# Kernel tuning notes

Measured on AMD Instinct MI355X. Metric: run time of the kernel, lower is better.

The kernel has to match this reference:

```python
import jax, jax.numpy as jnp
import numpy as np

B, S, D, H, L = 4, 2048, 512, 8, 4
DFF = 4 * D
CW = 128          # context_window
LS_MIN, LS_MAX = -6.0, 1.5


def setup_inputs() -> dict:
    key = jax.random.key(0)
    ks = jax.random.split(key, 10)
    s = 0.02
    p = lambda k, shape: jax.random.normal(k, shape, jnp.float32) * s
    return {
        "x": jax.random.normal(ks[0], (B, S, 2), jnp.float32),
        "W_in": p(ks[1], (D, 2)), "b_in": jnp.zeros((D,), jnp.float32),
        "pos": p(ks[2], (1, S, D)),
        "Wqkv": p(ks[3], (L, 3 * D, D)), "bqkv": jnp.zeros((L, 3 * D), jnp.float32),
        "Wo": p(ks[4], (L, D, D)), "bo": jnp.zeros((L, D), jnp.float32),
        "W1": p(ks[5], (L, DFF, D)), "b1": jnp.zeros((L, DFF), jnp.float32),
        "W2": p(ks[6], (L, D, DFF)), "b2": jnp.zeros((L, D), jnp.float32),
        "ln1_g": jnp.ones((L, D), jnp.float32), "ln1_b": jnp.zeros((L, D), jnp.float32),
        "ln2_g": jnp.ones((L, D), jnp.float32), "ln2_b": jnp.zeros((L, D), jnp.float32),
        "W_head": p(ks[7], (4, D)), "b_head": jnp.zeros((4,), jnp.float32),
    }


def _ln(x, g, b):
    m = x.mean(-1, keepdims=True)
    v = ((x - m) ** 2).mean(-1, keepdims=True)
    return (x - m) / jnp.sqrt(v + 1e-5) * g + b


def reference(x, W_in, b_in, pos, Wqkv, bqkv, Wo, bo, W1, b1, W2, b2,
              ln1_g, ln1_b, ln2_g, ln2_b, W_head, b_head):
    Bx, Sx, _ = x.shape
    h = x @ W_in.T + b_in + pos[:, :Sx, :]          # [B,S,D]
    idx = jnp.arange(Sx)
    # True = disallowed: future OR older than context window
    mask = (idx[None, :] > idx[:, None]) | (idx[None, :] < idx[:, None] - CW)
    dh = D // H
    scale = 1.0 / np.sqrt(dh).astype(np.float32)
    neg = jnp.float32(-1e30)
    for l in range(L):
        # self-attention (post-LN, as nn.TransformerEncoderLayer default)
        qkv = h @ Wqkv[l].T + bqkv[l]               # [B,S,3D]
        q, k, v = jnp.split(qkv, 3, axis=-1)
        q = q.reshape(Bx, Sx, H, dh)
        k = k.reshape(Bx, Sx, H, dh)
        v = v.reshape(Bx, Sx, H, dh)
        scores = jnp.einsum('bqhd,bkhd->bhqk', q, k) * scale
        scores = jnp.where(mask, neg, scores)
        attn = jax.nn.softmax(scores, axis=-1)
        o = jnp.einsum('bhqk,bkhd->bqhd', attn, v).reshape(Bx, Sx, D)
        h = _ln(h + o @ Wo[l].T + bo[l], ln1_g[l], ln1_b[l])
        # GELU FFN (exact erf gelu, torch default)
        ff = jax.nn.gelu(h @ W1[l].T + b1[l], approximate=False) @ W2[l].T + b2[l]
        h = _ln(h + ff, ln2_g[l], ln2_b[l])
    out = h @ W_head.T + b_head                     # [B,S,4]
    mu = out[..., :2]
    log_sigma = jnp.clip(out[..., 2:], LS_MIN, LS_MAX)
    return mu, log_sigma
```

## Files before the change

### kernel.cpp

```cpp
#include <hip/hip_runtime.h>
#include <hip/hip_bf16.h>
#include <math.h>

constexpr int Bc = 4;
constexpr int Sc = 2048;
constexpr int Dc = 512;
constexpr int Hc = 8;
constexpr int DHc = 64;
constexpr int Lc = 4;
constexpr int DFFc = 2048;
constexpr int Tc = Bc * Sc;
constexpr int QKVW = 3 * Dc;

typedef __attribute__((ext_vector_type(8))) short short8;
typedef __attribute__((ext_vector_type(4))) float f32x4;
typedef __attribute__((ext_vector_type(4))) float float4v;
typedef __attribute__((ext_vector_type(4))) unsigned int uint4v;

static __device__ __forceinline__ float u16tof(unsigned int u) {
  return __uint_as_float(u << 16);
}
static __device__ __forceinline__ unsigned short ftobf(float f) {
  __hip_bfloat16 h = __float2bfloat16(f);
  return *reinterpret_cast<unsigned short*>(&h);
}
static __device__ __forceinline__ void gload_lds16(const void* g, void* l) {
  __builtin_amdgcn_global_load_lds(
      (const __attribute__((address_space(1))) void*)g,
      (__attribute__((address_space(3))) void*)l, 16, 0, 0);
}

static __device__ __forceinline__ int swzK(int row, int col) {
  return row * 64 + ((((col >> 3) ^ (row & 7)) << 3) | (col & 7));
}
static __device__ __forceinline__ int swzW(int row, int col) {
  return row * 192 + ((((col >> 3) ^ (row & 7)) << 3) | (col & 7));
}

__global__ __launch_bounds__(256) void k_f2bf(const float* __restrict__ in,
                                              unsigned short* __restrict__ out,
                                              int n) {
  int i = blockIdx.x * 256 + threadIdx.x;
  if (i < n) out[i] = ftobf(in[i]);
}

__global__ __launch_bounds__(256) void k_embed(const float* __restrict__ x,
                                               const float* __restrict__ W_in,
                                               const float* __restrict__ b_in,
                                               const float* __restrict__ pos,
                                               float* __restrict__ h,
                                               unsigned short* __restrict__ hb) {
  int idx = blockIdx.x * 256 + threadIdx.x;
  int t = idx >> 9;
  int d = idx & 511;
  int s = t & (Sc - 1);
  float v = x[t * 2 + 0] * W_in[d * 2 + 0] + x[t * 2 + 1] * W_in[d * 2 + 1] +
            b_in[d] + pos[(size_t)s * Dc + d];
  h[idx] = v;
  hb[idx] = ftobf(v);
}

template <int MODE, int OUTBF>
__global__ __launch_bounds__(256, 4) void k_mgemm(const unsigned short* __restrict__ A,
                                                  const unsigned short* __restrict__ W,
                                                  const float* __restrict__ bias,
                                                  void* __restrict__ Cout,
                                                  int M, int N, int K) {
  __shared__ short SMEM[2][2][512 * 8];
  const int tid = threadIdx.x;
  const int lane = tid & 63;
  const int wid = tid >> 6;
  const int wm = wid >> 1;
  const int wn = wid & 1;

  const int nwg = gridDim.x * gridDim.y;
  const int bid = blockIdx.y * gridDim.x + blockIdx.x;
  const int swz = (bid & 7) * (nwg >> 3) + (bid >> 3);
  const int m0 = (swz / gridDim.x) * 128;
  const int n0 = (swz % gridDim.x) * 128;

  int r0S, c0S, r1S, c1S;
  {
    int p = tid;
    int rp = p >> 3, q = (p & 7) ^ (rp & 7);
    r0S = (rp << 1) | (q >> 2);
    c0S = q & 3;
    p = tid + 256;
    rp = p >> 3;
    q = (p & 7) ^ (rp & 7);
    r1S = (rp << 1) | (q >> 2);
    c1S = q & 3;
  }
  const unsigned short* a0p = A + (size_t)(m0 + r0S) * K + c0S * 8;
  const unsigned short* a1p = A + (size_t)(m0 + r1S) * K + c1S * 8;
  const unsigned short* b0p = W + (size_t)(n0 + r0S) * K + c0S * 8;
  const unsigned short* b1p = W + (size_t)(n0 + r1S) * K + c1S * 8;
  const int d0 = (tid & ~63) * 8;
  const int d1 = ((tid + 256) & ~63) * 8;

  f32x4 acc[4][4] = {};
  const int lr = lane & 15;
  const int chr = lane >> 4;

  gload_lds16(a0p, &SMEM[0][0][d0]);
  gload_lds16(a1p, &SMEM[0][0][d1]);
  gload_lds16(b0p, &SMEM[1][0][d0]);
  gload_lds16(b1p, &SMEM[1][0][d1]);
  __syncthreads();

  const int nsteps = K >> 5;
  int buf = 0;
  for (int s = 0; s < nsteps; ++s) {
    if (s + 1 < nsteps) {
      const int ko = (s + 1) << 5;
      gload_lds16(a0p + ko, &SMEM[0][buf ^ 1][d0]);
      gload_lds16(a1p + ko, &SMEM[0][buf ^ 1][d1]);
      gload_lds16(b0p + ko, &SMEM[1][buf ^ 1][d0]);
      gload_lds16(b1p + ko, &SMEM[1][buf ^ 1][d1]);
    }
    short8 af[4], bfr[4];
#pragma unroll
    for (int mi = 0; mi < 4; ++mi) {
      int row = wm * 64 + mi * 16 + lr;
      int rp = row >> 1;
      int p = rp * 8 + (((((row & 1) << 2) | chr)) ^ (rp & 7));
      af[mi] = *(const short8*)&SMEM[0][buf][p * 8];
    }
#pragma unroll
    for (int ni = 0; ni < 4; ++ni) {
      int row = wn * 64 + ni * 16 + lr;
      int rp = row >> 1;
      int p = rp * 8 + (((((row & 1) << 2) | chr)) ^ (rp & 7));
      bfr[ni] = *(const short8*)&SMEM[1][buf][p * 8];
    }
#pragma unroll
    for (int mi = 0; mi < 4; ++mi)
#pragma unroll
      for (int ni = 0; ni < 4; ++ni)
        acc[mi][ni] = __builtin_amdgcn_mfma_f32_16x16x32_bf16(
            af[mi], bfr[ni], acc[mi][ni], 0, 0, 0);
    __syncthreads();
    buf ^= 1;
  }

  float* cw = (float*)&SMEM[0][0][0] + wid * (16 * 68);
  const int cj = lane & 15;
  const int rj4 = (lane >> 4) * 4;
  const int rrd = lane >> 3;
  const int crd = (lane & 7) * 8;
#pragma unroll
  for (int mi = 0; mi < 4; ++mi) {
#pragma unroll
    for (int ni = 0; ni < 4; ++ni) {
      float bn = bias[n0 + wn * 64 + ni * 16 + cj];
#pragma unroll
      for (int j = 0; j < 4; ++j) {
        float v = acc[mi][ni][j] + bn;
        if (MODE == 2) v = 0.5f * v * (1.0f + erff(v * 0.70710678118654752f));
        cw[(rj4 + j) * 68 + ni * 16 + cj] = v;
      }
    }
    __builtin_amdgcn_sched_barrier(0);
#pragma unroll
    for (int t = 0; t < 2; ++t) {
      int rl = t * 8 + rrd;
      float4v v0 = *(const float4v*)&cw[rl * 68 + crd];
      float4v v1 = *(const float4v*)&cw[rl * 68 + crd + 4];
      size_t gbase = (size_t)(m0 + wm * 64 + mi * 16 + rl) * N +
                     (n0 + wn * 64 + crd);
      if (OUTBF) {
        unsigned int w0 = ftobf(v0[0]) | ((unsigned int)ftobf(v0[1]) << 16);
        unsigned int w1 = ftobf(v0[2]) | ((unsigned int)ftobf(v0[3]) << 16);
        unsigned int w2 = ftobf(v1[0]) | ((unsigned int)ftobf(v1[1]) << 16);
        unsigned int w3 = ftobf(v1[2]) | ((unsigned int)ftobf(v1[3]) << 16);
        uint4v pk = {w0, w1, w2, w3};
        *(uint4v*)&((unsigned short*)Cout)[gbase] = pk;
      } else {
        *(float4v*)&((float*)Cout)[gbase] = v0;
        *(float4v*)&((float*)Cout)[gbase + 4] = v1;
      }
    }
    __builtin_amdgcn_sched_barrier(0);
  }
}

__global__ __launch_bounds__(256, 3) void k_attn(const unsigned short* __restrict__ qkv,
                                                 unsigned short* __restrict__ o) {
  __shared__ unsigned short KPs[192 * 64];
  __shared__ unsigned short Vt[64 * 192];

  const int tid = threadIdx.x;
  const int lane = tid & 63;
  const int w = tid >> 6;
  const int idx = blockIdx.x;
  const int qb = idx & 31;
  const int hh = (idx >> 5) & 7;
  const int b = idx >> 8;
  const int q0 = qb * 64;
  const int kstart = max(0, q0 - 128);
  const int nk = q0 + 64 - kstart;

  for (int c = tid; c < nk * 8; c += 256) {
    int j = c >> 3, ch = c & 7;
    short8 kv = *(const short8*)&qkv[(size_t)(b * Sc + kstart + j) * QKVW + Dc + hh * DHc + ch * 8];
    *(short8*)&KPs[swzK(j, ch * 8)] = kv;
  }
  for (int c = tid; c < (nk >> 1) * 8; c += 256) {
    int jp = c >> 3, ch = c & 7;
    int j = jp * 2;
    const unsigned short* base =
        &qkv[(size_t)(b * Sc + kstart + j) * QKVW + 2 * Dc + hh * DHc + ch * 8];
    short8 v0 = *(const short8*)base;
    short8 v1 = *(const short8*)(base + QKVW);
#pragma unroll
    for (int i = 0; i < 8; ++i) {
      unsigned int pk = (unsigned short)v0[i] | ((unsigned int)(unsigned short)v1[i] << 16);
      *(unsigned int*)&Vt[swzW(ch * 8 + i, j)] = pk;
    }
  }
  if (nk < 192) {
    for (int c = tid; c < 64 * 64; c += 256) {
      int d = c >> 6, jo = c & 63;
      *(unsigned int*)&Vt[swzW(d, 64 + jo * 2)] = 0;
    }
  }

  const int qg = q0 + w * 16 + (lane & 15);
  const int kg8 = (lane >> 4) * 8;
  const unsigned short* qp = &qkv[(size_t)(b * Sc + qg) * QKVW + hh * DHc + kg8];
  short8 bq0 = *(const short8*)qp;
  short8 bq1 = *(const short8*)(qp + 32);
  __syncthreads();

  const int jb = max(0, q0 + w * 16 - 128) - kstart;

  f32x4 sacc[9];
#pragma unroll
  for (int t = 0; t < 9; ++t) {
    int key = jb + t * 16 + (lane & 15);
    short8 a0 = *(const short8*)&KPs[swzK(key, kg8)];
    short8 a1 = *(const short8*)&KPs[swzK(key, 32 + kg8)];
    f32x4 z = {0.f, 0.f, 0.f, 0.f};
    z = __builtin_amdgcn_mfma_f32_16x16x32_bf16(a0, bq0, z, 0, 0, 0);
    sacc[t] = __builtin_amdgcn_mfma_f32_16x16x32_bf16(a1, bq1, z, 0, 0, 0);
  }

  const int rj = (lane >> 4) * 4;
  float mx = -1e30f;
#pragma unroll
  for (int t = 0; t < 9; ++t) {
#pragma unroll
    for (int j = 0; j < 4; ++j) {
      int kglob = kstart + jb + t * 16 + rj + j;
      bool valid = (kglob <= qg) && (kglob + 128 >= qg);
      float s = valid ? sacc[t][j] * 0.125f : -1e30f;
      sacc[t][j] = s;
      mx = fmaxf(mx, s);
    }
  }
  mx = fmaxf(mx, __shfl_xor(mx, 16));
  mx = fmaxf(mx, __shfl_xor(mx, 32));
  float sum = 0.f;
#pragma unroll
  for (int t = 0; t < 9; ++t)
#pragma unroll
    for (int j = 0; j < 4; ++j) {
      float e = __expf(sacc[t][j] - mx);
      sacc[t][j] = e;
      sum += e;
    }
  sum += __shfl_xor(sum, 16);
  sum += __shfl_xor(sum, 32);
  const float inv = 1.0f / sum;

  __syncthreads();

  const int prow = w * 16 + (lane & 15);
#pragma unroll
  for (int t = 0; t < 9; ++t) {
    int c0 = jb + t * 16 + rj;
    unsigned int p0 = ftobf(sacc[t][0] * inv) |
                      ((unsigned int)ftobf(sacc[t][1] * inv) << 16);
    unsigned int p1 = ftobf(sacc[t][2] * inv) |
                      ((unsigned int)ftobf(sacc[t][3] * inv) << 16);
    *(unsigned int*)&KPs[swzW(prow, c0)] = p0;
    *(unsigned int*)&KPs[swzW(prow, c0 + 2)] = p1;
  }
  {
    int g2 = (lane >> 4) * 2;
    for (int col = g2; col < jb; col += 8)
      *(unsigned int*)&KPs[swzW(prow, col)] = 0;
    for (int col = jb + 144 + g2; col < 192; col += 8)
      *(unsigned int*)&KPs[swzW(prow, col)] = 0;
  }
  f32x4 oacc[4] = {};
#pragma unroll
  for (int kb = 0; kb < 6; ++kb) {
    short8 pa = *(const short8*)&KPs[swzW(prow, kb * 32 + kg8)];
#pragma unroll
    for (int dt = 0; dt < 4; ++dt) {
      short8 vb = *(const short8*)&Vt[swzW(dt * 16 + (lane & 15), kb * 32 + kg8)];
      oacc[dt] = __builtin_amdgcn_mfma_f32_16x16x32_bf16(pa, vb, oacc[dt], 0, 0, 0);
    }
  }
  const int cj = lane & 15;
#pragma unroll
  for (int j = 0; j < 4; ++j)
#pragma unroll
    for (int dt = 0; dt < 4; ++dt)
      o[(size_t)(b * Sc + q0 + w * 16 + rj + j) * Dc + hh * DHc + dt * 16 + cj] =
          ftobf(oacc[dt][j]);
}

__global__ __launch_bounds__(256) void k_lnr(float* __restrict__ h,
                                             const float* __restrict__ raw,
                                             const float* __restrict__ g,
                                             const float* __restrict__ bta,
                                             unsigned short* __restrict__ outb) {
  const int wid = threadIdx.x >> 6;
  const int lane = threadIdx.x & 63;
  const int t = blockIdx.x * 4 + wid;
  const float4v* hrow = (const float4v*)(h + (size_t)t * Dc);
  const float4v* rrow = (const float4v*)(raw + (size_t)t * Dc);
  float4v v[2];
  float sum = 0.0f, sq = 0.0f;
#pragma unroll
  for (int i = 0; i < 2; ++i) {
    float4v hv = hrow[lane + i * 64];
    float4v rv = rrow[lane + i * 64];
#pragma unroll
    for (int c = 0; c < 4; ++c) {
      float xv = rv[c] + hv[c];
      v[i][c] = xv;
      sum += xv;
      sq += xv * xv;
    }
  }
#pragma unroll
  for (int off = 32; off; off >>= 1) {
    sum += __shfl_xor(sum, off);
    sq += __shfl_xor(sq, off);
  }
  float m = sum * (1.0f / 512.0f);
  float var = sq * (1.0f / 512.0f) - m * m;
  float rstd = rsqrtf(var + 1e-5f);
  float4v* orow = (float4v*)(h + (size_t)t * Dc);
  unsigned int* brow = (unsigned int*)(outb + (size_t)t * Dc);
#pragma unroll
  for (int i = 0; i < 2; ++i) {
    int d4 = (lane + i * 64) * 4;
    float4v ov;
#pragma unroll
    for (int c = 0; c < 4; ++c)
      ov[c] = (v[i][c] - m) * rstd * g[d4 + c] + bta[d4 + c];
    orow[lane + i * 64] = ov;
    unsigned int p0 = ftobf(ov[0]) | ((unsigned int)ftobf(ov[1]) << 16);
    unsigned int p1 = ftobf(ov[2]) | ((unsigned int)ftobf(ov[3]) << 16);
    brow[(lane + i * 64) * 2] = p0;
    brow[(lane + i * 64) * 2 + 1] = p1;
  }
}

__global__ __launch_bounds__(256) void k_head(const float* __restrict__ h,
                                              const float* __restrict__ Wh,
                                              const float* __restrict__ bh,
                                              float* __restrict__ outp) {
  const int wid = threadIdx.x >> 6;
  const int lane = threadIdx.x & 63;
  const int t = blockIdx.x * 4 + wid;
  const float* row = h + (size_t)t * Dc;
  float a0 = 0, a1 = 0, a2 = 0, a3 = 0;
#pragma unroll
  for (int i = 0; i < 8; ++i) {
    int d = lane + i * 64;
    float xv = row[d];
    a0 += xv * Wh[0 * Dc + d];
    a1 += xv * Wh[1 * Dc + d];
    a2 += xv * Wh[2 * Dc + d];
    a3 += xv * Wh[3 * Dc + d];
  }
#pragma unroll
  for (int off = 32; off; off >>= 1) {
    a0 += __shfl_xor(a0, off);
    a1 += __shfl_xor(a1, off);
    a2 += __shfl_xor(a2, off);
    a3 += __shfl_xor(a3, off);
  }
  if (lane == 0) {
    outp[(size_t)t * 2 + 0] = a0 + bh[0];
    outp[(size_t)t * 2 + 1] = a1 + bh[1];
    outp[(size_t)Tc * 2 + (size_t)t * 2 + 0] = fminf(fmaxf(a2 + bh[2], -6.0f), 1.5f);
    outp[(size_t)Tc * 2 + (size_t)t * 2 + 1] = fminf(fmaxf(a3 + bh[3], -6.0f), 1.5f);
  }
}

extern "C" void kernel_launch(void* const* d_in, const int* in_sizes, int n_in,
                              void* d_out, int out_size, void* d_ws, size_t ws_size,
                              hipStream_t stream) {
  const float* x    = (const float*)d_in[0];
  const float* W_in = (const float*)d_in[1];
  const float* b_in = (const float*)d_in[2];
  const float* pos  = (const float*)d_in[3];
  const float* Wqkv = (const float*)d_in[4];
  const float* bqkv = (const float*)d_in[5];
  const float* Wo   = (const float*)d_in[6];
  const float* bo   = (const float*)d_in[7];
  const float* W1   = (const float*)d_in[8];
  const float* b1   = (const float*)d_in[9];
  const float* W2   = (const float*)d_in[10];
  const float* b2   = (const float*)d_in[11];
  const float* ln1g = (const float*)d_in[12];
  const float* ln1b = (const float*)d_in[13];
  const float* ln2g = (const float*)d_in[14];
  const float* ln2b = (const float*)d_in[15];
  const float* Wh   = (const float*)d_in[16];
  const float* bh   = (const float*)d_in[17];
  float* out = (float*)d_out;

  char* p = (char*)d_ws;
  float* h   = (float*)p;          p += (size_t)Tc * Dc * 4;
  float* t2  = (float*)p;          p += (size_t)Tc * Dc * 4;
  unsigned short* hb  = (unsigned short*)p; p += (size_t)Tc * Dc * 2;
  unsigned short* ob  = (unsigned short*)p; p += (size_t)Tc * Dc * 2;
  unsigned short* big = (unsigned short*)p; p += (size_t)Tc * DFFc * 2;
  unsigned short* wqb = (unsigned short*)p; p += (size_t)Lc * QKVW * Dc * 2;
  unsigned short* wob = (unsigned short*)p; p += (size_t)Lc * Dc * Dc * 2;
  unsigned short* w1b = (unsigned short*)p; p += (size_t)Lc * DFFc * Dc * 2;
  unsigned short* w2b = (unsigned short*)p; p += (size_t)Lc * Dc * DFFc * 2;

  k_f2bf<<<Lc * QKVW * Dc / 256, 256, 0, stream>>>(Wqkv, wqb, Lc * QKVW * Dc);
  k_f2bf<<<Lc * Dc * Dc / 256, 256, 0, stream>>>(Wo, wob, Lc * Dc * Dc);
  k_f2bf<<<Lc * DFFc * Dc / 256, 256, 0, stream>>>(W1, w1b, Lc * DFFc * Dc);
  k_f2bf<<<Lc * Dc * DFFc / 256, 256, 0, stream>>>(W2, w2b, Lc * Dc * DFFc);

  k_embed<<<(Tc * Dc) / 256, 256, 0, stream>>>(x, W_in, b_in, pos, h, hb);

  for (int l = 0; l < Lc; ++l) {
    const unsigned short* wq_l = wqb + (size_t)l * QKVW * Dc;
    const unsigned short* wo_l = wob + (size_t)l * Dc * Dc;
    const unsigned short* w1_l = w1b + (size_t)l * DFFc * Dc;
    const unsigned short* w2_l = w2b + (size_t)l * Dc * DFFc;

    k_mgemm<0, 1><<<dim3(QKVW / 128, Tc / 128), 256, 0, stream>>>(
        hb, wq_l, bqkv + (size_t)l * QKVW, big, Tc, QKVW, Dc);

    k_attn<<<Bc * Hc * (Sc / 64), 256, 0, stream>>>(big, ob);

    k_mgemm<0, 0><<<dim3(Dc / 128, Tc / 128), 256, 0, stream>>>(
        ob, wo_l, bo + (size_t)l * Dc, t2, Tc, Dc, Dc);

    k_lnr<<<Tc / 4, 256, 0, stream>>>(h, t2, ln1g + (size_t)l * Dc,
                                      ln1b + (size_t)l * Dc, hb);

    k_mgemm<2, 1><<<dim3(DFFc / 128, Tc / 128), 256, 0, stream>>>(
        hb, w1_l, b1 + (size_t)l * DFFc, big, Tc, DFFc, Dc);

    k_mgemm<0, 0><<<dim3(Dc / 128, Tc / 128), 256, 0, stream>>>(
        big, w2_l, b2 + (size_t)l * Dc, t2, Tc, Dc, DFFc);

    k_lnr<<<Tc / 4, 256, 0, stream>>>(h, t2, ln2g + (size_t)l * Dc,
                                      ln2b + (size_t)l * Dc, hb);
  }

  k_head<<<Tc / 4, 256, 0, stream>>>(h, Wh, bh, out);
}
```

Measured before the change: 606.0 us.

## Fuse output projection GEMM with residual LayerNorm and trim attention PV loop

Adds k_gln, a GEMM that computes full 512-wide rows for 16 tokens per block and applies bias, residual add and LayerNorm in its epilogue. It replaces the Wo GEMM plus separate k_lnr and drops the fp32 t2 round trip. The attention PV loop now skips 32-wide key blocks that are entirely zero, and the embedding kernel is vectorised to four elements per thread. The risk is that the 16-row tiles reload the full weight matrix from L2 for every block and give poor MFMA reuse, which may make the fused kernel slower than the larger-tile GEMM it replaces.

```diff
diff --git a/kernel.cpp b/kernel.cpp
--- a/kernel.cpp
+++ b/kernel.cpp
@@ -15,7 +15,9 @@
 typedef __attribute__((ext_vector_type(8))) short short8;
 typedef __attribute__((ext_vector_type(4))) float f32x4;
 typedef __attribute__((ext_vector_type(4))) float float4v;
+typedef __attribute__((ext_vector_type(2))) float float2v;
 typedef __attribute__((ext_vector_type(4))) unsigned int uint4v;
+typedef __attribute__((ext_vector_type(2))) unsigned int uint2v;
 
 static __device__ __forceinline__ float u16tof(unsigned int u) {
   return __uint_as_float(u << 16);
@@ -35,6 +37,9 @@
 }
 static __device__ __forceinline__ int swzW(int row, int col) {
   return row * 192 + ((((col >> 3) ^ (row & 7)) << 3) | (col & 7));
+}
+static __device__ __forceinline__ int gperm(int row, int ch) {
+  return (row >> 1) * 8 + (((((row & 1) << 2) | ch)) ^ ((row >> 1) & 7));
 }
 
 __global__ __launch_bounds__(256) void k_f2bf(const float* __restrict__ in,
@@ -50,14 +55,24 @@
                                                const float* __restrict__ pos,
                                                float* __restrict__ h,
                                                unsigned short* __restrict__ hb) {
-  int idx = blockIdx.x * 256 + threadIdx.x;
-  int t = idx >> 9;
-  int d = idx & 511;
+  int i4 = (blockIdx.x * 256 + threadIdx.x) * 4;
+  int t = i4 >> 9;
+  int d = i4 & 511;
   int s = t & (Sc - 1);
-  float v = x[t * 2 + 0] * W_in[d * 2 + 0] + x[t * 2 + 1] * W_in[d * 2 + 1] +
-            b_in[d] + pos[(size_t)s * Dc + d];
-  h[idx] = v;
-  hb[idx] = ftobf(v);
+  float x0 = x[t * 2 + 0], x1 = x[t * 2 + 1];
+  float4v w01 = *(const float4v*)&W_in[d * 2];
+  float4v w23 = *(const float4v*)&W_in[d * 2 + 4];
+  float4v pz = *(const float4v*)&pos[(size_t)s * Dc + d];
+  float4v b4 = *(const float4v*)&b_in[d];
+  float4v v;
+  v[0] = x0 * w01[0] + x1 * w01[1] + b4[0] + pz[0];
+  v[1] = x0 * w01[2] + x1 * w01[3] + b4[1] + pz[1];
+  v[2] = x0 * w23[0] + x1 * w23[1] + b4[2] + pz[2];
+  v[3] = x0 * w23[2] + x1 * w23[3] + b4[3] + pz[3];
+  *(float4v*)&h[i4] = v;
+  uint2v pk = {ftobf(v[0]) | ((unsigned int)ftobf(v[1]) << 16),
+               ftobf(v[2]) | ((unsigned int)ftobf(v[3]) << 16)};
+  *(uint2v*)&hb[i4] = pk;
 }
 
 template <int MODE, int OUTBF>
@@ -120,19 +135,11 @@
     }
     short8 af[4], bfr[4];
 #pragma unroll
-    for (int mi = 0; mi < 4; ++mi) {
-      int row = wm * 64 + mi * 16 + lr;
-      int rp = row >> 1;
-      int p = rp * 8 + (((((row & 1) << 2) | chr)) ^ (rp & 7));
-      af[mi] = *(const short8*)&SMEM[0][buf][p * 8];
-    }
-#pragma unroll
-    for (int ni = 0; ni < 4; ++ni) {
-      int row = wn * 64 + ni * 16 + lr;
-      int rp = row >> 1;
-      int p = rp * 8 + (((((row & 1) << 2) | chr)) ^ (rp & 7));
-      bfr[ni] = *(const short8*)&SMEM[1][buf][p * 8];
-    }
+    for (int mi = 0; mi < 4; ++mi)
+      af[mi] = *(const short8*)&SMEM[0][buf][gperm(wm * 64 + mi * 16 + lr, chr) * 8];
+#pragma unroll
+    for (int ni = 0; ni < 4; ++ni)
+      bfr[ni] = *(const short8*)&SMEM[1][buf][gperm(wn * 64 + ni * 16 + lr, chr) * 8];
 #pragma unroll
     for (int mi = 0; mi < 4; ++mi)
 #pragma unroll
@@ -184,6 +191,135 @@
   }
 }
 
+template <int KK>
+__global__ __launch_bounds__(256, 2) void k_gln(const unsigned short* __restrict__ A,
+                                                const unsigned short* __restrict__ W,
+                                                const float* __restrict__ bias,
+                                                const float* __restrict__ g,
+                                                const float* __restrict__ bta,
+                                                float* __restrict__ h,
+                                                unsigned short* __restrict__ hb) {
+  constexpr int NSTEP = KK / 32;
+  __shared__ unsigned short Bs[2][512 * 32];
+  __shared__ unsigned short As[2][16 * 32];
+  const int tid = threadIdx.x;
+  const int lane = tid & 63;
+  const int w = tid >> 6;
+
+  const int nwg = gridDim.x;
+  const int bid = blockIdx.x;
+  const int swz = (bid & 7) * (nwg >> 3) + (bid >> 3);
+  const int m0 = swz * 16;
+
+  const unsigned short* WpS[8];
+  int dstB[8];
+#pragma unroll
+  for (int i = 0; i < 8; ++i) {
+    int p = i * 256 + tid;
+    int rp = p >> 3, q = (p & 7) ^ (rp & 7);
+    int row = (rp << 1) | (q >> 2);
+    int ch = q & 3;
+    WpS[i] = W + (size_t)row * KK + ch * 8;
+    dstB[i] = ((i * 256 + tid) & ~63) * 8;
+  }
+  const int arow = tid >> 2, ach = tid & 3;
+  const unsigned short* ApS = A + (size_t)(m0 + arow) * KK + ach * 8;
+  const int apos = gperm(arow, ach) * 8;
+
+  f32x4 acc[8] = {};
+  const int lr = lane & 15;
+  const int chr = lane >> 4;
+
+#pragma unroll
+  for (int i = 0; i < 8; ++i) gload_lds16(WpS[i], &Bs[0][dstB[i]]);
+  short8 aval = {};
+  if (tid < 64) {
+    aval = *(const short8*)ApS;
+    *(short8*)&As[0][apos] = aval;
+    if (NSTEP > 1) aval = *(const short8*)(ApS + 32);
+  }
+  __syncthreads();
+
+  int buf = 0;
+  for (int s = 0; s < NSTEP; ++s) {
+    if (s + 1 < NSTEP) {
+      const int ko = (s + 1) << 5;
+#pragma unroll
+      for (int i = 0; i < 8; ++i) gload_lds16(WpS[i] + ko, &Bs[buf ^ 1][dstB[i]]);
+      if (tid < 64) {
+        *(short8*)&As[buf ^ 1][apos] = aval;
+        if (s + 2 < NSTEP) aval = *(const short8*)(ApS + ((s + 2) << 5));
+      }
+    }
+    short8 af = *(const short8*)&As[buf][gperm(lr, chr) * 8];
+    short8 bfr[8];
+#pragma unroll
+    for (int ni = 0; ni < 8; ++ni)
+      bfr[ni] = *(const short8*)&Bs[buf][gperm(w * 128 + ni * 16 + lr, chr) * 8];
+#pragma unroll
+    for (int ni = 0; ni < 8; ++ni)
+      acc[ni] = __builtin_amdgcn_mfma_f32_16x16x32_bf16(af, bfr[ni], acc[ni], 0, 0, 0);
+    __syncthreads();
+    buf ^= 1;
+  }
+
+  float* cw = (float*)&Bs[0][0];
+  const int cj = lane & 15;
+  const int rj4 = (lane >> 4) * 4;
+#pragma unroll
+  for (int ni = 0; ni < 8; ++ni) {
+    int col = w * 128 + ni * 16 + cj;
+    float bn = bias[col];
+#pragma unroll
+    for (int j = 0; j < 4; ++j)
+      cw[(rj4 + j) * 512 + col] = acc[ni][j] + bn;
+  }
+  __syncthreads();
+
+#pragma unroll
+  for (int r = 0; r < 4; ++r) {
+    const int row = w * 4 + r;
+    const size_t gm = (size_t)(m0 + row) * Dc;
+    float4v x0 = *(const float4v*)&cw[row * 512 + lane * 8];
+    float4v x1 = *(const float4v*)&cw[row * 512 + lane * 8 + 4];
+    float4v h0 = *(const float4v*)&h[gm + lane * 8];
+    float4v h1 = *(const float4v*)&h[gm + lane * 8 + 4];
+    float v[8];
+    float sum = 0.f, sq = 0.f;
+#pragma unroll
+    for (int c = 0; c < 4; ++c) {
+      v[c] = x0[c] + h0[c];
+      v[4 + c] = x1[c] + h1[c];
+    }
+#pragma unroll
+    for (int c = 0; c < 8; ++c) {
+      sum += v[c];
+      sq += v[c] * v[c];
+    }
+#pragma unroll
+    for (int off = 32; off; off >>= 1) {
+      sum += __shfl_xor(sum, off);
+      sq += __shfl_xor(sq, off);
+    }
+    float mu = sum * (1.0f / 512.0f);
+    float var = sq * (1.0f / 512.0f) - mu * mu;
+    float rstd = rsqrtf(var + 1e-5f);
+    float4v o0, o1;
+#pragma unroll
+    for (int c = 0; c < 4; ++c) {
+      o0[c] = (v[c] - mu) * rstd * g[lane * 8 + c] + bta[lane * 8 + c];
+      o1[c] = (v[4 + c] - mu) * rstd * g[lane * 8 + 4 + c] + bta[lane * 8 + 4 + c];
+    }
+    *(float4v*)&h[gm + lane * 8] = o0;
+    *(float4v*)&h[gm + lane * 8 + 4] = o1;
+    uint4v pk = {ftobf(o0[0]) | ((unsigned int)ftobf(o0[1]) << 16),
+                 ftobf(o0[2]) | ((unsigned int)ftobf(o0[3]) << 16),
+                 ftobf(o1[0]) | ((unsigned int)ftobf(o1[1]) << 16),
+                 ftobf(o1[2]) | ((unsigned int)ftobf(o1[3]) << 16)};
+    *(uint4v*)&hb[gm + lane * 8] = pk;
+  }
+}
+
 __global__ __launch_bounds__(256, 3) void k_attn(const unsigned short* __restrict__ qkv,
                                                  unsigned short* __restrict__ o) {
   __shared__ unsigned short KPs[192 * 64];
@@ -293,9 +429,10 @@
     for (int col = jb + 144 + g2; col < 192; col += 8)
       *(unsigned int*)&KPs[swzW(prow, col)] = 0;
   }
+  const int kb0 = jb >> 5;
+  const int kbend = min(6, (jb + 144 + 31) >> 5);
   f32x4 oacc[4] = {};
-#pragma unroll
-  for (int kb = 0; kb < 6; ++kb) {
+  for (int kb = kb0; kb < kbend; ++kb) {
     short8 pa = *(const short8*)&KPs[swzW(prow, kb * 32 + kg8)];
 #pragma unroll
     for (int dt = 0; dt < 4; ++dt) {
@@ -433,7 +570,7 @@
   k_f2bf<<<Lc * DFFc * Dc / 256, 256, 0, stream>>>(W1, w1b, Lc * DFFc * Dc);
   k_f2bf<<<Lc * Dc * DFFc / 256, 256, 0, stream>>>(W2, w2b, Lc * Dc * DFFc);
 
-  k_embed<<<(Tc * Dc) / 256, 256, 0, stream>>>(x, W_in, b_in, pos, h, hb);
+  k_embed<<<(Tc * Dc) / 1024, 256, 0, stream>>>(x, W_in, b_in, pos, h, hb);
 
   for (int l = 0; l < Lc; ++l) {
     const unsigned short* wq_l = wqb + (size_t)l * QKVW * Dc;
@@ -446,11 +583,9 @@
 
     k_attn<<<Bc * Hc * (Sc / 64), 256, 0, stream>>>(big, ob);
 
-    k_mgemm<0, 0><<<dim3(Dc / 128, Tc / 128), 256, 0, stream>>>(
-        ob, wo_l, bo + (size_t)l * Dc, t2, Tc, Dc, Dc);
-
-    k_lnr<<<Tc / 4, 256, 0, stream>>>(h, t2, ln1g + (size_t)l * Dc,
-                                      ln1b + (size_t)l * Dc, hb);
+    k_gln<Dc><<<Tc / 16, 256, 0, stream>>>(
+        ob, wo_l, bo + (size_t)l * Dc, ln1g + (size_t)l * Dc,
+        ln1b + (size_t)l * Dc, h, hb);
 
     k_mgemm<2, 1><<<dim3(DFFc / 128, Tc / 128), 256, 0, stream>>>(
         hb, w1_l, b1 + (size_t)l * DFFc, big, Tc, DFFc, Dc);
```

Measured after the change: 613.2 us. About the same (+1.2%).
